# Performance work log

Hardware: AMD Instinct MI355X
Metric: run time of the kernel (lower is better)

The kernel has to match this reference:

```python
import jax, jax.numpy as jnp
import numpy as np

EPS = 1e-5  # torch nn.LayerNorm default eps
DIST_CUTOFF = 10.0


def _ln(x, g, b):
    m = jnp.mean(x, axis=-1, keepdims=True)
    v = jnp.mean((x - m) ** 2, axis=-1, keepdims=True)
    return (x - m) * jax.lax.rsqrt(v + EPS) * g + b


def setup_inputs() -> dict:
    key = jax.random.key(0)
    ks = iter(jax.random.split(key, 48))
    L, B, N, D, H = 4, 1, 256, 128, 512
    IN = D + N  # 384 == node_dim + edge_dim + node_dim under the consistency constraint
    r = lambda *s: jax.random.normal(next(ks), s, jnp.float32) * 0.02
    return dict(
        nodes=jax.random.normal(next(ks), (B, N, D), jnp.float32),
        coords=jax.random.normal(next(ks), (B, N, 3), jnp.float32),
        ee_w=r(1, D), ee_b=jnp.zeros(D), ee_g=jnp.ones(D), ee_bt=jnp.zeros(D),
        nu1_w=r(L, IN, H), nu1_b=jnp.zeros((L, H)), nu_g=jnp.ones((L, H)), nu_bt=jnp.zeros((L, H)),
        nu2_w=r(L, H, D), nu2_b=jnp.zeros((L, D)),
        eu1_w=r(L, IN, H), eu1_b=jnp.zeros((L, H)), eu_g=jnp.ones((L, H)), eu_bt=jnp.zeros((L, H)),
        eu2_w=r(L, H, D), eu2_b=jnp.zeros((L, D)),
        sp1_w=r(D, H), sp1_b=jnp.zeros(H), sp_g=jnp.ones(H), sp_bt=jnp.zeros(H),
        sp2_w=r(H, 3), sp2_b=jnp.zeros(3),
        no1_w=r(D, H), no1_b=jnp.zeros(H), no_g=jnp.ones(H), no_bt=jnp.zeros(H),
        no2_w=r(H, D), no2_b=jnp.zeros(D),
    )


def reference(nodes, coords, ee_w, ee_b, ee_g, ee_bt,
              nu1_w, nu1_b, nu_g, nu_bt, nu2_w, nu2_b,
              eu1_w, eu1_b, eu_g, eu_bt, eu2_w, eu2_b,
              sp1_w, sp1_b, sp_g, sp_bt, sp2_w, sp2_b,
              no1_w, no1_b, no_g, no_bt, no2_w, no2_b):
    B, N, D = nodes.shape
    # initialize_edges: pairwise distances -> edge embedding + adjacency
    diff = coords[:, :, None, :] - coords[:, None, :, :]           # [B,N,N,3]
    sq = jnp.sum(diff * diff, axis=-1)                              # [B,N,N]
    dist = jnp.where(sq > 0, jnp.sqrt(jnp.where(sq > 0, sq, 1.0)), 0.0)
    adj = (dist < DIST_CUTOFF).astype(nodes.dtype)                  # [B,N,N]
    edges = jax.nn.relu(_ln(dist[..., None] @ ee_w + ee_b, ee_g, ee_bt))  # [B,N,N,D]

    def step(carry, p):
        nd, ed = carry
        w1n, b1n, gn, btn, w2n, b2n, w1e, b1e, ge, bte, w2e, b2e = p
        # messages: einsum('bijk,bik->bij', edges*adj[...,None], nodes)
        msgs = adj * jnp.einsum('bijk,bik->bij', ed, nd)            # [B,N,N]
        ni = jnp.concatenate([nd, msgs], axis=-1)                    # [B,N,D+N]
        nd_new = nd + jax.nn.relu(_ln(ni @ w1n + b1n, gn, btn)) @ w2n + b2n
        pairs = jnp.concatenate([
            jnp.broadcast_to(nd[:, :, None, :], (B, N, N, D)),
            jnp.broadcast_to(nd[:, None, :, :], (B, N, N, D))], axis=-1)  # [B,N,N,2D]
        ei = jnp.concatenate([ed, pairs], axis=-1)                   # [B,N,N,3D]
        ed_new = ed + jax.nn.relu(_ln(ei @ w1e + b1e, ge, bte)) @ w2e + b2e
        return (nd_new, ed_new), None

    (nd, _ed), _ = jax.lax.scan(
        step, (nodes, edges),
        (nu1_w, nu1_b, nu_g, nu_bt, nu2_w, nu2_b,
         eu1_w, eu1_b, eu_g, eu_bt, eu2_w, eu2_b))

    nodes_out = jax.nn.relu(_ln(nd @ no1_w + no1_b, no_g, no_bt)) @ no2_w + no2_b
    coords_pred = jax.nn.relu(_ln(nodes_out @ sp1_w + sp1_b, sp_g, sp_bt)) @ sp2_w + sp2_b
    return nodes_out, coords_pred
```

## Files before the change

### kernel.cpp

```cpp
#include <hip/hip_runtime.h>

#define LNEPS 1e-5f

typedef unsigned short ushort_t;
typedef __attribute__((ext_vector_type(8))) short short8;
typedef __attribute__((ext_vector_type(4))) float f32x4;

__device__ inline unsigned short f2b(float f) {
    union { float f; unsigned int u; } c; c.f = f;
    unsigned int u = c.u;
    unsigned int r = (u + 0x7FFFu + ((u >> 16) & 1u)) >> 16;
    return (unsigned short)r;
}

__global__ void k_convw(const float* __restrict__ w1, const float* __restrict__ w2,
                        ushort_t* __restrict__ w1P, ushort_t* __restrict__ w2P) {
    int idx = blockIdx.x * 256 + threadIdx.x;
    if (idx < 65536) {
        int l = idx >> 14, r = idx & 16383;
        int c = r >> 9;  r &= 511;
        int kb = r >> 6, lane = r & 63;
        int col = c * 16 + (lane & 15);
        int k0 = kb * 32 + (lane >> 4) * 8;
        ushort_t o[8];
        #pragma unroll
        for (int e = 0; e < 8; ++e) {
            int kl = k0 + e;
            int row = kl < 128 ? kl : kl + 128;
            o[e] = f2b(w1[((size_t)l * 384 + row) * 512 + col]);
        }
        *(uint4*)(w1P + (size_t)idx * 8) = *(uint4*)o;
    }
    if (idx < 32768) {
        int l = idx >> 13, r = idx & 8191;
        int c2 = r >> 10; r &= 1023;
        int kbg = r >> 6, lane = r & 63;
        int col = c2 * 16 + (lane & 15);
        int k0 = kbg * 32 + (lane >> 4) * 8;
        ushort_t o[8];
        #pragma unroll
        for (int e = 0; e < 8; ++e)
            o[e] = f2b(w2[((size_t)l * 512 + k0 + e) * 128 + col]);
        *(uint4*)(w2P + (size_t)idx * 8) = *(uint4*)o;
    }
}

__global__ void k_init(const float* __restrict__ coords, const float* __restrict__ nodes,
                       const float* __restrict__ ee_w, const float* __restrict__ ee_b,
                       const float* __restrict__ ee_g, const float* __restrict__ ee_bt,
                       float* __restrict__ ed, ushort_t* __restrict__ edb,
                       float* __restrict__ adjf, float* __restrict__ msgs) {
    int r = blockIdx.x * 4 + (threadIdx.x >> 6);
    int lane = threadIdx.x & 63;
    int i = r >> 8, j = r & 255;
    float dx = coords[i * 3 + 0] - coords[j * 3 + 0];
    float dy = coords[i * 3 + 1] - coords[j * 3 + 1];
    float dz = coords[i * 3 + 2] - coords[j * 3 + 2];
    float sq = dx * dx + dy * dy + dz * dz;
    float dist = sq > 0.f ? sqrtf(sq) : 0.f;
    float adjv = dist < 10.f ? 1.f : 0.f;
    if (lane == 0) adjf[r] = adjv;
    float e0 = dist * ee_w[lane] + ee_b[lane];
    float e1 = dist * ee_w[lane + 64] + ee_b[lane + 64];
    float s = e0 + e1, q = e0 * e0 + e1 * e1;
    #pragma unroll
    for (int off = 1; off < 64; off <<= 1) {
        s += __shfl_xor(s, off, 64);
        q += __shfl_xor(q, off, 64);
    }
    float mean = s * (1.f / 128.f);
    float var = q * (1.f / 128.f) - mean * mean;
    float rs = rsqrtf(var + LNEPS);
    float e0r = fmaxf((e0 - mean) * rs * ee_g[lane] + ee_bt[lane], 0.f);
    float e1r = fmaxf((e1 - mean) * rs * ee_g[lane + 64] + ee_bt[lane + 64], 0.f);
    ed[(size_t)r * 128 + lane]       = e0r;
    ed[(size_t)r * 128 + lane + 64]  = e1r;
    edb[(size_t)r * 128 + lane]      = f2b(e0r);
    edb[(size_t)r * 128 + lane + 64] = f2b(e1r);
    float d = e0r * nodes[(i << 7) + lane] + e1r * nodes[(i << 7) + 64 + lane];
    #pragma unroll
    for (int off = 1; off < 64; off <<= 1) d += __shfl_xor(d, off, 64);
    if (lane == 0) msgs[r] = adjv * d;
}

__global__ __launch_bounds__(512) void k_node(
    const float* __restrict__ nd, const float* __restrict__ msgs,
    const float* __restrict__ W1n, const float* __restrict__ b1n,
    const float* __restrict__ gn, const float* __restrict__ btn,
    const float* __restrict__ W2n, const float* __restrict__ b2n,
    float* __restrict__ ndout,
    const float* __restrict__ W1e, const float* __restrict__ b1e,
    float* __restrict__ cI, ushort_t* __restrict__ ndb) {
    __shared__ float ni[512];
    __shared__ float hsh[512];
    __shared__ float part[4][128];
    __shared__ float red[16];
    int t = threadIdx.x;
    if (blockIdx.x >= 256) {
        int p = blockIdx.x - 256;
        if (t < 128) {
            float v = nd[(size_t)p * 128 + t];
            ni[t] = v;
            ndb[(size_t)p * 128 + t] = f2b(v);
        }
        __syncthreads();
        const float* wm = W1e + (size_t)128 * 512 + t;
        float a1 = b1e[t];
        #pragma unroll 4
        for (int k = 0; k < 128; ++k) a1 += ni[k] * wm[(size_t)k * 512];
        cI[(size_t)p * 512 + t] = a1;
        return;
    }
    int row = blockIdx.x;
    if (t < 128) ni[t] = nd[(size_t)row * 128 + t];
    else if (t < 384) ni[t] = msgs[(size_t)row * 256 + (t - 128)];
    __syncthreads();
    float acc = b1n[t];
    #pragma unroll 4
    for (int k = 0; k < 384; ++k) acc += ni[k] * W1n[(size_t)k * 512 + t];
    float s = acc, q = acc * acc;
    #pragma unroll
    for (int off = 1; off < 64; off <<= 1) {
        s += __shfl_xor(s, off, 64);
        q += __shfl_xor(q, off, 64);
    }
    int wv = t >> 6;
    if ((t & 63) == 0) { red[wv] = s; red[8 + wv] = q; }
    __syncthreads();
    float S = 0.f, Q = 0.f;
    #pragma unroll
    for (int w = 0; w < 8; ++w) { S += red[w]; Q += red[8 + w]; }
    float mean = S * (1.f / 512.f);
    float var = Q * (1.f / 512.f) - mean * mean;
    float rs = rsqrtf(var + LNEPS);
    hsh[t] = fmaxf((acc - mean) * rs * gn[t] + btn[t], 0.f);
    __syncthreads();
    int qd = t >> 7, c = t & 127;
    float pacc = 0.f;
    #pragma unroll 4
    for (int kk = 0; kk < 128; ++kk)
        pacc += hsh[qd * 128 + kk] * W2n[(size_t)(qd * 128 + kk) * 128 + c];
    part[qd][c] = pacc;
    __syncthreads();
    if (t < 128) {
        float v = part[0][t] + part[1][t] + part[2][t] + part[3][t] + b2n[t]
                + nd[(size_t)row * 128 + t];
        ndout[(size_t)row * 128 + t] = v;
    }
}

__global__ __launch_bounds__(512) void k_mlp(
    const float* __restrict__ in0, int w0,
    const float* __restrict__ W1, const float* __restrict__ b1,
    const float* __restrict__ g, const float* __restrict__ bt,
    const float* __restrict__ W2, const float* __restrict__ b2, int O,
    float* __restrict__ out) {
    __shared__ float ni[384];
    __shared__ float hsh[512];
    __shared__ float part[4][128];
    __shared__ float red[16];
    int row = blockIdx.x;
    int t = threadIdx.x;
    if (t < w0) ni[t] = in0[(size_t)row * w0 + t];
    __syncthreads();
    float acc = b1[t];
    #pragma unroll 4
    for (int k = 0; k < w0; ++k) acc += ni[k] * W1[(size_t)k * 512 + t];
    float s = acc, q = acc * acc;
    #pragma unroll
    for (int off = 1; off < 64; off <<= 1) {
        s += __shfl_xor(s, off, 64);
        q += __shfl_xor(q, off, 64);
    }
    int wv = t >> 6;
    if ((t & 63) == 0) { red[wv] = s; red[8 + wv] = q; }
    __syncthreads();
    float S = 0.f, Q = 0.f;
    #pragma unroll
    for (int w = 0; w < 8; ++w) { S += red[w]; Q += red[8 + w]; }
    float mean = S * (1.f / 512.f);
    float var = Q * (1.f / 512.f) - mean * mean;
    float rs = rsqrtf(var + LNEPS);
    hsh[t] = fmaxf((acc - mean) * rs * g[t] + bt[t], 0.f);
    __syncthreads();
    int qd = t >> 7, c = t & 127;
    float pacc = 0.f;
    if (c < O) {
        #pragma unroll 4
        for (int kk = 0; kk < 128; ++kk)
            pacc += hsh[qd * 128 + kk] * W2[(size_t)(qd * 128 + kk) * O + c];
    }
    part[qd][c] = pacc;
    __syncthreads();
    if (t < O) {
        float v = part[0][t] + part[1][t] + part[2][t] + part[3][t] + b2[t];
        out[(size_t)row * O + t] = v;
    }
}

__global__ __launch_bounds__(512, 4) void k_edge(
    float* ed, ushort_t* edb, const ushort_t* __restrict__ ndb,
    const float* __restrict__ cIg, const ushort_t* __restrict__ w1P,
    const float* __restrict__ g, const float* __restrict__ bt,
    const ushort_t* __restrict__ w2P, const float* __restrict__ b2,
    const float* __restrict__ ndn, const float* __restrict__ adjf,
    float* __restrict__ msgs) {
    __shared__ char smem[37376];
    const int tid = threadIdx.x;
    const int w = tid >> 6, lane = tid & 63;
    const int l15 = lane & 15, lhi = lane >> 4;
    const int rbase = blockIdx.x * 64;
    const int ib = rbase >> 8;
    const int jbase = rbase & 255;

    #pragma unroll
    for (int it = 0; it < 4; ++it) {
        int c = tid + it * 512;
        int row = c >> 5, q = c & 31;
        uint4 pk;
        if (q < 16) pk = *(const uint4*)(edb + (size_t)(rbase + row) * 128 + q * 8);
        else        pk = *(const uint4*)(ndb + (size_t)(jbase + row) * 128 + (q - 16) * 8);
        *(uint4*)(smem + row * 512 + ((q ^ (row & 7)) * 16)) = pk;
    }
    __syncthreads();

    f32x4 acc[4][4];
    f32x4 zero = {0.f, 0.f, 0.f, 0.f};
    #pragma unroll
    for (int m = 0; m < 4; ++m)
        #pragma unroll
        for (int n = 0; n < 4; ++n) acc[m][n] = zero;

    const int cw = w * 64;
    #pragma unroll 4
    for (int kb = 0; kb < 8; ++kb) {
        short8 a[4];
        #pragma unroll
        for (int m = 0; m < 4; ++m) {
            int row = m * 16 + l15;
            a[m] = *(const short8*)(smem + row * 512 + (((kb * 4 + lhi) ^ (row & 7)) * 16));
        }
        #pragma unroll
        for (int n = 0; n < 4; ++n) {
            short8 b = *(const short8*)(w1P + ((((w * 4 + n) * 8 + kb) << 6) + lane) * 8);
            #pragma unroll
            for (int m = 0; m < 4; ++m)
                acc[m][n] = __builtin_amdgcn_mfma_f32_16x16x32_bf16(b, a[m], acc[m][n], 0, 0, 0);
        }
    }

    float* red = (float*)(smem + 32768);
    float* stats = (float*)(smem + 36864);
    {
        float4 ci[4];
        #pragma unroll
        for (int n = 0; n < 4; ++n)
            ci[n] = *(const float4*)(cIg + (size_t)ib * 512 + cw + n * 16 + lhi * 4);
        #pragma unroll
        for (int m = 0; m < 4; ++m) {
            float s = 0.f, q = 0.f;
            #pragma unroll
            for (int n = 0; n < 4; ++n) {
                float v0 = acc[m][n][0] + ci[n].x;
                float v1 = acc[m][n][1] + ci[n].y;
                float v2 = acc[m][n][2] + ci[n].z;
                float v3 = acc[m][n][3] + ci[n].w;
                acc[m][n][0] = v0; acc[m][n][1] = v1;
                acc[m][n][2] = v2; acc[m][n][3] = v3;
                s += v0 + v1 + v2 + v3;
                q += v0 * v0 + v1 * v1 + v2 * v2 + v3 * v3;
            }
            s += __shfl_xor(s, 16, 64);
            s += __shfl_xor(s, 32, 64);
            q += __shfl_xor(q, 16, 64);
            q += __shfl_xor(q, 32, 64);
            if (lhi == 0) {
                red[(w * 64 + m * 16 + l15) * 2 + 0] = s;
                red[(w * 64 + m * 16 + l15) * 2 + 1] = q;
            }
        }
    }
    __syncthreads();
    if (tid < 64) {
        float S = 0.f, Q = 0.f;
        #pragma unroll
        for (int ww = 0; ww < 8; ++ww) {
            S += red[(ww * 64 + tid) * 2 + 0];
            Q += red[(ww * 64 + tid) * 2 + 1];
        }
        float mean = S * (1.f / 512.f);
        float var = Q * (1.f / 512.f) - mean * mean;
        stats[tid * 2 + 0] = mean;
        stats[tid * 2 + 1] = rsqrtf(var + LNEPS);
    }
    __syncthreads();

    {
        float4 gg[4], bb[4];
        #pragma unroll
        for (int n = 0; n < 4; ++n) {
            gg[n] = *(const float4*)(g + cw + n * 16 + lhi * 4);
            bb[n] = *(const float4*)(bt + cw + n * 16 + lhi * 4);
        }
        #pragma unroll
        for (int m = 0; m < 4; ++m) {
            int row = m * 16 + l15;
            float mean = stats[row * 2 + 0];
            float rs = stats[row * 2 + 1];
            #pragma unroll
            for (int n = 0; n < 4; ++n) {
                acc[m][n][0] = fmaxf((acc[m][n][0] - mean) * rs * gg[n].x + bb[n].x, 0.f);
                acc[m][n][1] = fmaxf((acc[m][n][1] - mean) * rs * gg[n].y + bb[n].y, 0.f);
                acc[m][n][2] = fmaxf((acc[m][n][2] - mean) * rs * gg[n].z + bb[n].z, 0.f);
                acc[m][n][3] = fmaxf((acc[m][n][3] - mean) * rs * gg[n].w + bb[n].w, 0.f);
            }
        }
    }

    const int rt = w >> 1, ch2 = w & 1;
    const int arow = rt * 16 + l15;
    f32x4 acc2[4];
    #pragma unroll
    for (int n2 = 0; n2 < 4; ++n2) acc2[n2] = zero;

    #pragma unroll
    for (int hf = 0; hf < 2; ++hf) {
        if ((w >> 2) == hf) {
            const int base = (w & 3) * 64;
            #pragma unroll
            for (int m = 0; m < 4; ++m) {
                int row = m * 16 + l15;
                #pragma unroll
                for (int n = 0; n < 4; ++n) {
                    int p0 = base + n * 16 + lhi * 4;
                    int addr = row * 512 + ((((p0 >> 3) ^ (row & 7))) * 16) + (p0 & 7) * 2;
                    uint2 pk;
                    pk.x = (unsigned)f2b(acc[m][n][0]) | ((unsigned)f2b(acc[m][n][1]) << 16);
                    pk.y = (unsigned)f2b(acc[m][n][2]) | ((unsigned)f2b(acc[m][n][3]) << 16);
                    *(uint2*)(smem + addr) = pk;
                }
            }
        }
        __syncthreads();
        #pragma unroll 2
        for (int kbg = 0; kbg < 8; ++kbg) {
            short8 a = *(const short8*)(smem + arow * 512 + (((kbg * 4 + lhi) ^ (arow & 7)) * 16));
            #pragma unroll
            for (int n2 = 0; n2 < 4; ++n2) {
                short8 b = *(const short8*)(w2P + ((((ch2 * 4 + n2) * 16 + hf * 8 + kbg) << 6) + lane) * 8);
                acc2[n2] = __builtin_amdgcn_mfma_f32_16x16x32_bf16(b, a, acc2[n2], 0, 0, 0);
            }
        }
        __syncthreads();
    }

    float partial = 0.f;
    {
        const int row = rt * 16 + l15;
        #pragma unroll
        for (int n2 = 0; n2 < 4; ++n2) {
            int col0 = ch2 * 64 + n2 * 16 + lhi * 4;
            size_t goff = (size_t)(rbase + row) * 128 + col0;
            float4 r4 = *(const float4*)(ed + goff);
            float4 b4 = *(const float4*)(b2 + col0);
            float4 n4 = *(const float4*)(ndn + (size_t)ib * 128 + col0);
            float o0 = acc2[n2][0] + b4.x + r4.x;
            float o1 = acc2[n2][1] + b4.y + r4.y;
            float o2 = acc2[n2][2] + b4.z + r4.z;
            float o3 = acc2[n2][3] + b4.w + r4.w;
            float4 o4 = {o0, o1, o2, o3};
            *(float4*)(ed + goff) = o4;
            uint2 pk;
            pk.x = (unsigned)f2b(o0) | ((unsigned)f2b(o1) << 16);
            pk.y = (unsigned)f2b(o2) | ((unsigned)f2b(o3) << 16);
            *(uint2*)(edb + goff) = pk;
            partial += o0 * n4.x + o1 * n4.y + o2 * n4.z + o3 * n4.w;
        }
    }
    partial += __shfl_xor(partial, 16, 64);
    partial += __shfl_xor(partial, 32, 64);
    float* msum = (float*)(smem + 32768);
    if (lhi == 0) msum[ch2 * 64 + rt * 16 + l15] = partial;
    __syncthreads();
    if (tid < 64) msgs[rbase + tid] = adjf[rbase + tid] * (msum[tid] + msum[64 + tid]);
}

extern "C" void kernel_launch(void* const* d_in, const int* in_sizes, int n_in,
                              void* d_out, int out_size, void* d_ws, size_t ws_size,
                              hipStream_t stream) {
    const float* nodes  = (const float*)d_in[0];
    const float* coords = (const float*)d_in[1];
    const float* ee_w   = (const float*)d_in[2];
    const float* ee_b   = (const float*)d_in[3];
    const float* ee_g   = (const float*)d_in[4];
    const float* ee_bt  = (const float*)d_in[5];
    const float* nu1_w  = (const float*)d_in[6];
    const float* nu1_b  = (const float*)d_in[7];
    const float* nu_g   = (const float*)d_in[8];
    const float* nu_bt  = (const float*)d_in[9];
    const float* nu2_w  = (const float*)d_in[10];
    const float* nu2_b  = (const float*)d_in[11];
    const float* eu1_w  = (const float*)d_in[12];
    const float* eu1_b  = (const float*)d_in[13];
    const float* eu_g   = (const float*)d_in[14];
    const float* eu_bt  = (const float*)d_in[15];
    const float* eu2_w  = (const float*)d_in[16];
    const float* eu2_b  = (const float*)d_in[17];
    const float* sp1_w  = (const float*)d_in[18];
    const float* sp1_b  = (const float*)d_in[19];
    const float* sp_g   = (const float*)d_in[20];
    const float* sp_bt  = (const float*)d_in[21];
    const float* sp2_w  = (const float*)d_in[22];
    const float* sp2_b  = (const float*)d_in[23];
    const float* no1_w  = (const float*)d_in[24];
    const float* no1_b  = (const float*)d_in[25];
    const float* no_g   = (const float*)d_in[26];
    const float* no_bt  = (const float*)d_in[27];
    const float* no2_w  = (const float*)d_in[28];
    const float* no2_b  = (const float*)d_in[29];

    char* p = (char*)d_ws;
    float* ed      = (float*)p;     p += (size_t)65536 * 128 * 4;
    ushort_t* edb  = (ushort_t*)p;  p += (size_t)65536 * 128 * 2;
    float* ndA     = (float*)p;     p += 256 * 128 * 4;
    float* ndB     = (float*)p;     p += 256 * 128 * 4;
    ushort_t* ndb  = (ushort_t*)p;  p += 256 * 128 * 2;
    float* msgs    = (float*)p;     p += 65536 * 4;
    float* adjf    = (float*)p;     p += 65536 * 4;
    float* cI      = (float*)p;     p += 256 * 512 * 4;
    ushort_t* w1P  = (ushort_t*)p;  p += (size_t)4 * 131072 * 2;
    ushort_t* w2P  = (ushort_t*)p;  p += (size_t)4 * 65536 * 2;

    k_convw<<<256, 256, 0, stream>>>(eu1_w, eu2_w, w1P, w2P);
    k_init<<<16384, 256, 0, stream>>>(coords, nodes, ee_w, ee_b, ee_g, ee_bt,
                                      ed, edb, adjf, msgs);

    const float* nd_cur = nodes;
    float* nd_bufs[2] = {ndA, ndB};
    for (int l = 0; l < 4; ++l) {
        float* nd_next = nd_bufs[l & 1];
        k_node<<<512, 512, 0, stream>>>(nd_cur, msgs,
            nu1_w + (size_t)l * 384 * 512, nu1_b + l * 512, nu_g + l * 512, nu_bt + l * 512,
            nu2_w + (size_t)l * 512 * 128, nu2_b + l * 128, nd_next,
            eu1_w + (size_t)l * 384 * 512, eu1_b + l * 512, cI, ndb);
        k_edge<<<1024, 512, 0, stream>>>(ed, edb, ndb, cI,
            w1P + (size_t)l * 131072, eu_g + l * 512, eu_bt + l * 512,
            w2P + (size_t)l * 65536, eu2_b + l * 128,
            nd_next, adjf, msgs);
        nd_cur = nd_next;
    }

    float* out_nodes  = (float*)d_out;
    float* out_coords = out_nodes + 32768;
    k_mlp<<<256, 512, 0, stream>>>(nd_cur, 128,
        no1_w, no1_b, no_g, no_bt, no2_w, no2_b, 128, out_nodes);
    k_mlp<<<256, 512, 0, stream>>>(out_nodes, 128,
        sp1_w, sp1_b, sp_g, sp_bt, sp2_w, sp2_b, 3, out_coords);
}
```

Measured before the change: 654.7 us.

## Stage full hidden tile in LDS and coalesce edge epilogue via shared staging

The edge kernel now writes the whole 64x512 bf16 hidden activation into a doubled LDS buffer in one pass, replacing the two-half staging with its extra barriers, so the second GEMM runs as a single 16-step K loop. The output tile is then staged through LDS as fp32 so each thread reads, writes and converts 16 contiguous elements. This gives wide coalesced global accesses for the residual, fp32 and bf16 edge stores, and the message reduction becomes an 8-lane shuffle. The cost is LDS use rising from about 37KB to about 70KB per block, which may cut how many blocks fit per CU below the launch-bounds target of 4.

```diff
diff --git a/kernel.cpp b/kernel.cpp
--- a/kernel.cpp
+++ b/kernel.cpp
@@ -205,7 +205,7 @@
     const ushort_t* __restrict__ w2P, const float* __restrict__ b2,
     const float* __restrict__ ndn, const float* __restrict__ adjf,
     float* __restrict__ msgs) {
-    __shared__ char smem[37376];
+    __shared__ char smem[70144];
     const int tid = threadIdx.x;
     const int w = tid >> 6, lane = tid & 63;
     const int l15 = lane & 15, lhi = lane >> 4;
@@ -232,7 +232,7 @@
         for (int n = 0; n < 4; ++n) acc[m][n] = zero;
 
     const int cw = w * 64;
-    #pragma unroll 4
+    #pragma unroll 2
     for (int kb = 0; kb < 8; ++kb) {
         short8 a[4];
         #pragma unroll
@@ -249,8 +249,8 @@
         }
     }
 
-    float* red = (float*)(smem + 32768);
-    float* stats = (float*)(smem + 36864);
+    float* red = (float*)(smem + 65536);
+    float* stats = (float*)(smem + 69632);
     {
         float4 ci[4];
         #pragma unroll
@@ -309,80 +309,90 @@
             float rs = stats[row * 2 + 1];
             #pragma unroll
             for (int n = 0; n < 4; ++n) {
-                acc[m][n][0] = fmaxf((acc[m][n][0] - mean) * rs * gg[n].x + bb[n].x, 0.f);
-                acc[m][n][1] = fmaxf((acc[m][n][1] - mean) * rs * gg[n].y + bb[n].y, 0.f);
-                acc[m][n][2] = fmaxf((acc[m][n][2] - mean) * rs * gg[n].z + bb[n].z, 0.f);
-                acc[m][n][3] = fmaxf((acc[m][n][3] - mean) * rs * gg[n].w + bb[n].w, 0.f);
+                float v0 = fmaxf((acc[m][n][0] - mean) * rs * gg[n].x + bb[n].x, 0.f);
+                float v1 = fmaxf((acc[m][n][1] - mean) * rs * gg[n].y + bb[n].y, 0.f);
+                float v2 = fmaxf((acc[m][n][2] - mean) * rs * gg[n].z + bb[n].z, 0.f);
+                float v3 = fmaxf((acc[m][n][3] - mean) * rs * gg[n].w + bb[n].w, 0.f);
+                int p0 = cw + n * 16 + lhi * 4;
+                int addr = row * 1024 + ((((p0 >> 3) ^ (row & 7))) * 16) + (p0 & 7) * 2;
+                uint2 pk;
+                pk.x = (unsigned)f2b(v0) | ((unsigned)f2b(v1) << 16);
+                pk.y = (unsigned)f2b(v2) | ((unsigned)f2b(v3) << 16);
+                *(uint2*)(smem + addr) = pk;
             }
         }
     }
+    __syncthreads();
 
     const int rt = w >> 1, ch2 = w & 1;
+    f32x4 acc2[4];
+    #pragma unroll
+    for (int n2 = 0; n2 < 4; ++n2) acc2[n2] = zero;
     const int arow = rt * 16 + l15;
-    f32x4 acc2[4];
-    #pragma unroll
-    for (int n2 = 0; n2 < 4; ++n2) acc2[n2] = zero;
-
-    #pragma unroll
-    for (int hf = 0; hf < 2; ++hf) {
-        if ((w >> 2) == hf) {
-            const int base = (w & 3) * 64;
-            #pragma unroll
-            for (int m = 0; m < 4; ++m) {
-                int row = m * 16 + l15;
-                #pragma unroll
-                for (int n = 0; n < 4; ++n) {
-                    int p0 = base + n * 16 + lhi * 4;
-                    int addr = row * 512 + ((((p0 >> 3) ^ (row & 7))) * 16) + (p0 & 7) * 2;
-                    uint2 pk;
-                    pk.x = (unsigned)f2b(acc[m][n][0]) | ((unsigned)f2b(acc[m][n][1]) << 16);
-                    pk.y = (unsigned)f2b(acc[m][n][2]) | ((unsigned)f2b(acc[m][n][3]) << 16);
-                    *(uint2*)(smem + addr) = pk;
-                }
-            }
-        }
-        __syncthreads();
-        #pragma unroll 2
-        for (int kbg = 0; kbg < 8; ++kbg) {
-            short8 a = *(const short8*)(smem + arow * 512 + (((kbg * 4 + lhi) ^ (arow & 7)) * 16));
-            #pragma unroll
-            for (int n2 = 0; n2 < 4; ++n2) {
-                short8 b = *(const short8*)(w2P + ((((ch2 * 4 + n2) * 16 + hf * 8 + kbg) << 6) + lane) * 8);
-                acc2[n2] = __builtin_amdgcn_mfma_f32_16x16x32_bf16(b, a, acc2[n2], 0, 0, 0);
-            }
-        }
-        __syncthreads();
-    }
-
-    float partial = 0.f;
+    #pragma unroll 2
+    for (int kbg = 0; kbg < 16; ++kbg) {
+        short8 a = *(const short8*)(smem + arow * 1024 + (((kbg * 4 + lhi) ^ (arow & 7)) * 16));
+        #pragma unroll
+        for (int n2 = 0; n2 < 4; ++n2) {
+            short8 b = *(const short8*)(w2P + ((((ch2 * 4 + n2) * 16 + kbg) << 6) + lane) * 8);
+            acc2[n2] = __builtin_amdgcn_mfma_f32_16x16x32_bf16(b, a, acc2[n2], 0, 0, 0);
+        }
+    }
+    __syncthreads();
+
+    float* outs = (float*)smem;
     {
         const int row = rt * 16 + l15;
         #pragma unroll
         for (int n2 = 0; n2 < 4; ++n2) {
             int col0 = ch2 * 64 + n2 * 16 + lhi * 4;
-            size_t goff = (size_t)(rbase + row) * 128 + col0;
-            float4 r4 = *(const float4*)(ed + goff);
             float4 b4 = *(const float4*)(b2 + col0);
-            float4 n4 = *(const float4*)(ndn + (size_t)ib * 128 + col0);
-            float o0 = acc2[n2][0] + b4.x + r4.x;
-            float o1 = acc2[n2][1] + b4.y + r4.y;
-            float o2 = acc2[n2][2] + b4.z + r4.z;
-            float o3 = acc2[n2][3] + b4.w + r4.w;
-            float4 o4 = {o0, o1, o2, o3};
-            *(float4*)(ed + goff) = o4;
-            uint2 pk;
-            pk.x = (unsigned)f2b(o0) | ((unsigned)f2b(o1) << 16);
-            pk.y = (unsigned)f2b(o2) | ((unsigned)f2b(o3) << 16);
-            *(uint2*)(edb + goff) = pk;
-            partial += o0 * n4.x + o1 * n4.y + o2 * n4.z + o3 * n4.w;
-        }
-    }
-    partial += __shfl_xor(partial, 16, 64);
-    partial += __shfl_xor(partial, 32, 64);
-    float* msum = (float*)(smem + 32768);
-    if (lhi == 0) msum[ch2 * 64 + rt * 16 + l15] = partial;
-    __syncthreads();
-    if (tid < 64) msgs[rbase + tid] = adjf[rbase + tid] * (msum[tid] + msum[64 + tid]);
+            float4 o4 = {acc2[n2][0] + b4.x, acc2[n2][1] + b4.y,
+                         acc2[n2][2] + b4.z, acc2[n2][3] + b4.w};
+            *(float4*)(outs + (size_t)row * 132 + col0) = o4;
+        }
+    }
+    __syncthreads();
+
+    {
+        const int row = tid >> 3, col0 = (tid & 7) * 16;
+        const size_t goff = (size_t)(rbase + row) * 128 + col0;
+        const float* src = outs + (size_t)row * 132 + col0;
+        const float* nsr = ndn + (size_t)ib * 128 + col0;
+        float o[16];
+        float partial = 0.f;
+        #pragma unroll
+        for (int c = 0; c < 4; ++c) {
+            float4 s4 = *(const float4*)(src + c * 4);
+            float4 r4 = *(const float4*)(ed + goff + c * 4);
+            float4 n4 = *(const float4*)(nsr + c * 4);
+            o[c * 4 + 0] = s4.x + r4.x;
+            o[c * 4 + 1] = s4.y + r4.y;
+            o[c * 4 + 2] = s4.z + r4.z;
+            o[c * 4 + 3] = s4.w + r4.w;
+            partial += o[c * 4 + 0] * n4.x + o[c * 4 + 1] * n4.y
+                     + o[c * 4 + 2] * n4.z + o[c * 4 + 3] * n4.w;
+            *(float4*)(ed + goff + c * 4) = *(float4*)(o + c * 4);
+        }
+        uint4 pk0, pk1;
+        pk0.x = (unsigned)f2b(o[0])  | ((unsigned)f2b(o[1])  << 16);
+        pk0.y = (unsigned)f2b(o[2])  | ((unsigned)f2b(o[3])  << 16);
+        pk0.z = (unsigned)f2b(o[4])  | ((unsigned)f2b(o[5])  << 16);
+        pk0.w = (unsigned)f2b(o[6])  | ((unsigned)f2b(o[7])  << 16);
+        pk1.x = (unsigned)f2b(o[8])  | ((unsigned)f2b(o[9])  << 16);
+        pk1.y = (unsigned)f2b(o[10]) | ((unsigned)f2b(o[11]) << 16);
+        pk1.z = (unsigned)f2b(o[12]) | ((unsigned)f2b(o[13]) << 16);
+        pk1.w = (unsigned)f2b(o[14]) | ((unsigned)f2b(o[15]) << 16);
+        *(uint4*)(edb + goff)     = pk0;
+        *(uint4*)(edb + goff + 8) = pk1;
+        partial += __shfl_xor(partial, 1, 64);
+        partial += __shfl_xor(partial, 2, 64);
+        partial += __shfl_xor(partial, 4, 64);
+        float* msum = (float*)(smem + 65536);
+        if ((tid & 7) == 0) msum[row] = partial;
+        __syncthreads();
+        if (tid < 64) msgs[rbase + tid] = adjf[rbase + tid] * msum[tid];
+    }
 }
 
 extern "C" void kernel_launch(void* const* d_in, const int* in_sizes, int n_in,
```

Measured after the change: 611.3 us. -6.6%, faster.
